# Optimization experiments

Hardware: AMD Instinct MI355X
Metric: run time of the kernel (lower is better)

The kernel has to match this reference:

```python
import jax, jax.numpy as jnp
import numpy as np

N, A, C, H, W = 2, 9, 80, 100, 152
STRIDE = 8
IM_H, IM_W = float(H * STRIDE), float(W * STRIDE)
PRE_NMS_THRESH = 0.05
PRE_NMS_TOP_N = 1000
NMS_THRESH = 0.5
POST_TOP_N = 100
MIN_SIZE = 0.0
WX = WY = 10.0
WW = WH = 5.0
BBOX_XFORM_CLIP = float(np.log(1000.0 / 16.0))
CLS_OFFSET = 4096.0  # > max image coord, makes per-class NMS equivalent


def _make_anchors():
    # 3 scales x 3 ratios, base size 32 at stride 8 (FPN P3)
    sizes = 32.0 * np.array([1.0, 2.0 ** (1.0 / 3.0), 2.0 ** (2.0 / 3.0)])
    ratios = np.array([0.5, 1.0, 2.0])
    ws, hs = [], []
    for s in sizes:
        for r in ratios:
            ws.append(s * np.sqrt(1.0 / r))
            hs.append(s * np.sqrt(r))
    ws = np.array(ws)  # [A]
    hs = np.array(hs)
    sx = (np.arange(W) + 0.5) * STRIDE
    sy = (np.arange(H) + 0.5) * STRIDE
    cx, cy = np.meshgrid(sx, sy)  # [H, W]
    cx = cx.reshape(-1, 1)
    cy = cy.reshape(-1, 1)
    x1 = cx - 0.5 * ws
    y1 = cy - 0.5 * hs
    x2 = cx + 0.5 * ws
    y2 = cy + 0.5 * hs
    # layout matches permute_and_flatten: index = (h*W + w)*A + a
    return np.stack([x1, y1, x2, y2], -1).reshape(-1, 4).astype(np.float32)


def setup_inputs() -> dict:
    key = jax.random.key(0)
    k1, k2 = jax.random.split(key)
    # shift logits down so sigmoid scores are mostly below pre_nms_thresh (realistic sparsity)
    box_cls = jax.random.normal(k1, (N, A * C, H, W), dtype=jnp.float32) * 2.0 - 4.0
    box_regression = jax.random.normal(k2, (N, A * 4, H, W), dtype=jnp.float32)
    anchors = jnp.asarray(_make_anchors())  # [H*W*A, 4]
    return {"box_cls": box_cls, "box_regression": box_regression, "anchors": anchors}


def _decode(rel, anc):
    # BoxCoder(weights=(10,10,5,5)).decode, TO_REMOVE = 1
    widths = anc[..., 2] - anc[..., 0] + 1.0
    heights = anc[..., 3] - anc[..., 1] + 1.0
    ctr_x = anc[..., 0] + 0.5 * widths
    ctr_y = anc[..., 1] + 0.5 * heights
    dx = rel[..., 0] / WX
    dy = rel[..., 1] / WY
    dw = jnp.minimum(rel[..., 2] / WW, BBOX_XFORM_CLIP)
    dh = jnp.minimum(rel[..., 3] / WH, BBOX_XFORM_CLIP)
    pcx = dx * widths + ctr_x
    pcy = dy * heights + ctr_y
    pw = jnp.exp(dw) * widths
    ph = jnp.exp(dh) * heights
    return jnp.stack(
        [pcx - 0.5 * pw, pcy - 0.5 * ph, pcx + 0.5 * pw - 1.0, pcy + 0.5 * ph - 1.0], -1)


def _nms_keep(boxes, scores, valid):
    # greedy NMS over boxes already sorted by score desc; returns bool keep [K]
    x1, y1, x2, y2 = boxes[:, 0], boxes[:, 1], boxes[:, 2], boxes[:, 3]
    areas = (x2 - x1 + 1.0) * (y2 - y1 + 1.0)
    iw = jnp.maximum(jnp.minimum(x2[:, None], x2[None, :]) - jnp.maximum(x1[:, None], x1[None, :]) + 1.0, 0.0)
    ih = jnp.maximum(jnp.minimum(y2[:, None], y2[None, :]) - jnp.maximum(y1[:, None], y1[None, :]) + 1.0, 0.0)
    inter = iw * ih
    iou = inter / (areas[:, None] + areas[None, :] - inter)  # [K, K]
    K = boxes.shape[0]

    def step(supp, i):
        ki = valid[i] & jnp.logical_not(supp[i])
        supp = supp | jnp.where(ki, iou[i] > NMS_THRESH, False)
        return supp, ki

    _, keep = jax.lax.scan(step, jnp.zeros(K, dtype=bool), jnp.arange(K))
    return keep


def reference(box_cls, box_regression, anchors):
    n = box_cls.shape[0]
    # permute_and_flatten: [N, A*C, H, W] -> [N, H*W*A, C], then sigmoid
    scores = jax.nn.sigmoid(
        box_cls.reshape(n, A, C, H, W).transpose(0, 3, 4, 1, 2).reshape(n, H * W * A, C))
    regs = box_regression.reshape(n, A, 4, H, W).transpose(0, 3, 4, 1, 2).reshape(n, H * W * A, 4)
    # threshold + capped top-k over flattened (anchor, class) pairs
    masked = jnp.where(scores > PRE_NMS_THRESH, scores, -1.0).reshape(n, -1)
    top_scores, top_idx = jax.lax.top_k(masked, PRE_NMS_TOP_N)  # sorted desc
    loc = top_idx // C            # anchor location
    labels = top_idx % C + 1      # per_class += 1
    valid = top_scores > 0.0      # padded slots have score -1
    reg_sel = jnp.take_along_axis(regs, loc[..., None], axis=1)  # [N, K, 4]
    anc_sel = anchors[loc]                                       # [N, K, 4]
    boxes = _decode(reg_sel, anc_sel)
    # clip_to_image
    x1 = jnp.clip(boxes[..., 0], 0.0, IM_W - 1.0)
    y1 = jnp.clip(boxes[..., 1], 0.0, IM_H - 1.0)
    x2 = jnp.clip(boxes[..., 2], 0.0, IM_W - 1.0)
    y2 = jnp.clip(boxes[..., 3], 0.0, IM_H - 1.0)
    boxes = jnp.stack([x1, y1, x2, y2], -1)
    # remove_small_boxes (TO_REMOVE = 1)
    valid = valid & (x2 - x1 + 1.0 >= MIN_SIZE) & (y2 - y1 + 1.0 >= MIN_SIZE)
    # per-class NMS via class-offset trick (boxes of different classes never overlap)
    off = labels.astype(boxes.dtype)[..., None] * CLS_OFFSET
    keep = jax.vmap(_nms_keep)(boxes + off, top_scores, valid)
    kept_scores = jnp.where(keep & valid, top_scores, -1.0)
    # select_over_all_levels: keep top fpn_post_nms_top_n by score
    final_scores, fidx = jax.lax.top_k(kept_scores, POST_TOP_N)
    final_boxes = jnp.take_along_axis(boxes, fidx[..., None], axis=1)
    final_labels = jnp.where(final_scores > 0.0, jnp.take_along_axis(labels, fidx, axis=1), 0)
    return final_boxes, final_scores, final_labels
```

## Files before the change

kernel.cpp:

```cpp
#include <hip/hip_runtime.h>


#define W_    152
#define H_    100
#define A_    9
#define C_    80
#define HW_   (H_*W_)
#define PER_IMG  (A_*C_*HW_)
#define PER_IMG4 (PER_IMG/4)
#define NBIN  2048
#define BIGA_CAP 4096
#define SORTN 2048
#define FASTN 1024
#define NDEC  256
#define THRB 2.0f
#define THRA 3.65f
#define CLIPV 4.135166556742356f

#define TPB      256
#define F4_BATCH 16
#define NBATCH   2
#define CHUNK    (TPB*F4_BATCH*NBATCH)
#define NB_SCAN  ((PER_IMG4 + CHUNK - 1) / CHUNK)
#define LCAPA 64

#define OFF_CNTA 0
#define OFF_DONE 8
#define OFF_DEC  256
#define OFF_BIGA (256 + 24576)

typedef unsigned long long u64;

__global__ __launch_bounds__(TPB) void scan_kernel(
    const float* __restrict__ cls,
    unsigned int* __restrict__ cntA,
    u64* __restrict__ bigA) {
  const int n = blockIdx.y;
  const float4* __restrict__ in = reinterpret_cast<const float4*>(cls) + (size_t)n * PER_IMG4;
  __shared__ unsigned int lcntA, lbaseA;
  __shared__ u64 lkA[LCAPA];
  if (threadIdx.x == 0) lcntA = 0;
  __syncthreads();

#pragma unroll
  for (int half = 0; half < NBATCH; ++half) {
    const int hbase = blockIdx.x * CHUNK + half * (TPB * F4_BATCH) + threadIdx.x;
    float4 v[F4_BATCH];
#pragma unroll
    for (int j = 0; j < F4_BATCH; ++j) {
      const int t = hbase + j * TPB;
      v[j] = (t < PER_IMG4) ? in[t]
                            : make_float4(-100.f, -100.f, -100.f, -100.f);
    }
#pragma unroll
    for (int j = 0; j < F4_BATCH; ++j) {
      const float4 vv = v[j];
      const float mx = fmaxf(fmaxf(vv.x, vv.y), fmaxf(vv.z, vv.w));
      if (mx > THRA) {
        const int f0  = (hbase + j * TPB) * 4;
        const int ac  = f0 / HW_;
        const int rem = f0 - ac * HW_;
        const int h   = rem / W_;
        const int w0  = rem - h * W_;
        const int a   = ac / C_;
        const int c   = ac - a * C_;
        const int idx0 = ((h * W_ + w0) * A_ + a) * C_ + c;
        const float xs[4] = {vv.x, vv.y, vv.z, vv.w};
#pragma unroll
        for (int e = 0; e < 4; ++e) {
          const float x = xs[e];
          if (x > THRA) {
            float s = 1.0f / (1.0f + expf(-x));
            unsigned pa = atomicAdd(&lcntA, 1u);
            if (pa < LCAPA)
              lkA[pa] = ((u64)__float_as_uint(s) << 32) |
                        (u64)(0xFFFFFFFFu - (unsigned)(idx0 + e * 720));
          }
        }
      }
    }
  }
  __syncthreads();
  if (threadIdx.x == 0) {
    unsigned cA = lcntA; if (cA > LCAPA) cA = LCAPA;
    lbaseA = cA ? atomicAdd(&cntA[n], cA) : 0u;
    lcntA = cA;
  }
  __syncthreads();
  if (threadIdx.x < lcntA) {
    unsigned pos = lbaseA + threadIdx.x;
    if (pos < BIGA_CAP)
      bigA[(size_t)n * BIGA_CAP + pos] = lkA[threadIdx.x];
  }
}

__device__ __forceinline__ void decode_box(
    int idx, float sc, int n,
    const float* __restrict__ reg, const float* __restrict__ anchors,
    float4& o0, float4& o1, float4& o2) {
  int c   = idx % C_;
  int loc = idx / C_;
  int a   = loc % A_;
  int hw  = loc / A_;
  int hh  = hw / W_;
  int ww  = hw - hh * W_;
  int rb  = ((n * A_ + a) * 4) * HW_ + hh * W_ + ww;
  float r0 = reg[rb], r1 = reg[rb + HW_], r2 = reg[rb + 2*HW_], r3 = reg[rb + 3*HW_];
  float4 an = reinterpret_cast<const float4*>(anchors)[loc];
  float wdt = an.z - an.x + 1.0f, hgt = an.w - an.y + 1.0f;
  float cx  = an.x + 0.5f * wdt, cy = an.y + 0.5f * hgt;
  float dx = r0 / 10.0f, dy = r1 / 10.0f;
  float dw = fminf(r2 / 5.0f, CLIPV), dh = fminf(r3 / 5.0f, CLIPV);
  float pcx = dx * wdt + cx, pcy = dy * hgt + cy;
  float pw = expf(dw) * wdt, ph = expf(dh) * hgt;
  float x1 = pcx - 0.5f * pw, y1 = pcy - 0.5f * ph;
  float x2 = pcx + 0.5f * pw - 1.0f, y2 = pcy + 0.5f * ph - 1.0f;
  x1 = fminf(fmaxf(x1, 0.0f), (float)(W_*8) - 1.0f);
  y1 = fminf(fmaxf(y1, 0.0f), (float)(H_*8) - 1.0f);
  x2 = fminf(fmaxf(x2, 0.0f), (float)(W_*8) - 1.0f);
  y2 = fminf(fmaxf(y2, 0.0f), (float)(H_*8) - 1.0f);
  bool valid = sc > 0.0f;
  if ((x2 - x1 + 1.0f < 0.0f) || (y2 - y1 + 1.0f < 0.0f)) valid = false;
  int   label = c + 1;
  float off = (float)label * 4096.0f;
  float ox1 = x1 + off, oy1 = y1 + off, ox2 = x2 + off, oy2 = y2 + off;
  o0 = make_float4(ox1, oy1, ox2, oy2);
  o1 = make_float4(x1, y1, x2, y2);
  o2 = make_float4((ox2 - ox1 + 1.0f) * (oy2 - oy1 + 1.0f),
                   valid ? sc : -1.0f, (float)label, 0.0f);
}

__global__ __launch_bounds__(256) void rank_nms_kernel(
    const float* __restrict__ cls,
    const unsigned int* __restrict__ cntA,
    const u64* __restrict__ bigA,
    const float* __restrict__ reg, const float* __restrict__ anchors,
    unsigned int* __restrict__ done,
    float4* __restrict__ dec,
    float* __restrict__ out) {
  const int n = blockIdx.x >> 5;
  const int b = blockIdx.x & 31;
  const int tid = threadIdx.x;
  const int lane = tid & 63;

  __shared__ u64 skl[FASTN];
  __shared__ int s_last;
  __shared__ float4 dall[3 * NDEC];
  __shared__ int s_fb, s_k, s_cut, s_cnt;
  __shared__ int keptidx[100];
  __shared__ u64 skey[SORTN];
  __shared__ unsigned int shist[NBIN];
  __shared__ unsigned int csum[256];
  __shared__ float4 fb0[1000], fb1[1000], fb2[1000];
  __shared__ unsigned char skeep[1000];

  const int caRaw = (int)cntA[n];
  int ca = caRaw; if (ca > FASTN) ca = FASTN;

#pragma unroll
  for (int r = 0; r < 4; ++r) {
    int j = tid + r * 256;
    skl[j] = (j < ca) ? bigA[(size_t)n * BIGA_CAP + j] : 0ull;
  }
  __syncthreads();

  const int kidx = b * 32 + (tid >> 3);
  const int sub  = tid & 7;
  const u64 ki = skl[kidx];
  int rank = 0;
#pragma unroll 8
  for (int it = 0; it < 128; ++it) {
    int j = sub + it * 8;
    u64 kj = skl[j];
    rank += (int)((kj > ki) | ((kj == ki) & (j < kidx)));
  }
  rank += __shfl_xor(rank, 1);
  rank += __shfl_xor(rank, 2);
  rank += __shfl_xor(rank, 4);
  if (sub == 0 && rank < NDEC && ki != 0ull) {
    int idx = (int)(0xFFFFFFFFu - (unsigned)(ki & 0xFFFFFFFFu));
    float sc = __uint_as_float((unsigned)(ki >> 32));
    float4 o0, o1, o2;
    decode_box(idx, sc, n, reg, anchors, o0, o1, o2);
    float4* d = dec + (size_t)n * (3 * NDEC);
    d[rank]            = o0;
    d[NDEC + rank]     = o1;
    d[2 * NDEC + rank] = o2;
  }

  __threadfence();
  if (tid == 0) {
    unsigned old = atomicAdd(&done[n], 1u);
    s_last = (old == 31u) ? 1 : 0;
  }
  __syncthreads();
  if (!s_last) return;
  __threadfence();

  if (tid == 0) { s_cnt = 0; s_fb = (caRaw > FASTN || caRaw < NDEC) ? 1 : 0; }

  if (caRaw >= NDEC && caRaw <= FASTN) {
#pragma unroll
    for (int r = 0; r < 3; ++r)
      dall[tid + r * 256] = dec[(size_t)n * (3 * NDEC) + tid + r * 256];
  }
  __syncthreads();

  float4* d0 = dall;
  float4* d1 = dall + NDEC;
  float4* d2 = dall + 2 * NDEC;

  if (s_fb == 0) {
    if (tid < 64) {
      float ka_x1 = 0, ka_y1 = 0, ka_x2 = 0, ka_y2 = 0, ka_ar = 0;
      float kb_x1 = 0, kb_y1 = 0, kb_x2 = 0, kb_y2 = 0, kb_ar = 0;
      int k = 0;
      for (int i = 0; i < NDEC; ++i) {
        if (k >= 100) break;
        float4 bx = d0[i];
        float4 ai = d2[i];
        float x1 = bx.x, y1 = bx.y, x2 = bx.z, y2 = bx.w, ar = ai.x, sc = ai.y;
        bool sup = false;
        if (lane < k) {
          float iw = fminf(x2, ka_x2) - fmaxf(x1, ka_x1) + 1.0f;
          float ih = fminf(y2, ka_y2) - fmaxf(y1, ka_y1) + 1.0f;
          if (iw > 0.0f && ih > 0.0f) {
            float inter = iw * ih;
            sup = inter / (ar + ka_ar - inter) > 0.5f;
          }
        }
        if (lane + 64 < k) {
          float iw = fminf(x2, kb_x2) - fmaxf(x1, kb_x1) + 1.0f;
          float ih = fminf(y2, kb_y2) - fmaxf(y1, kb_y1) + 1.0f;
          if (iw > 0.0f && ih > 0.0f) {
            float inter = iw * ih;
            sup = sup || (inter / (ar + kb_ar - inter) > 0.5f);
          }
        }
        bool any = __any(sup);
        if ((sc > 0.0f) && !any) {
          if (lane == k)      { ka_x1 = x1; ka_y1 = y1; ka_x2 = x2; ka_y2 = y2; ka_ar = ar; }
          if (lane == k - 64) { kb_x1 = x1; kb_y1 = y1; kb_x2 = x2; kb_y2 = y2; kb_ar = ar; }
          if (lane == 0) keptidx[k] = i;
          ++k;
        }
      }
      if (lane == 0) {
        s_k = k;
        if (k < 100) s_fb = 1;
      }
    }
    __syncthreads();

    if (s_fb == 0) {
      if (tid < 100) {
        int f = keptidx[tid];
        float4 bb = d1[f];
        float4 ai = d2[f];
        int ob = (n * 100 + tid) * 4;
        out[ob + 0] = bb.x; out[ob + 1] = bb.y; out[ob + 2] = bb.z; out[ob + 3] = bb.w;
        out[800  + n * 100 + tid] = ai.y;
        out[1000 + n * 100 + tid] = ai.z;
      }
      return;
    }
  }
  __syncthreads();

  for (int i = tid; i < NBIN; i += 256) shist[i] = 0;
  __syncthreads();
  const float* __restrict__ cn = cls + (size_t)n * PER_IMG;
  for (int e = tid; e < PER_IMG; e += 256) {
    float x = cn[e];
    if (x > THRB) {
      int bb = (int)((x - THRB) * 256.0f); if (bb > NBIN - 1) bb = NBIN - 1;
      atomicAdd(&shist[bb], 1u);
    }
  }
  __syncthreads();
  {
    unsigned int s = 0;
    for (int bb = tid * 8; bb < tid * 8 + 8; ++bb) s += shist[bb];
    csum[tid] = s;
  }
  __syncthreads();
  if (tid == 0) {
    int acc = 0, cut = 0;
    for (int cch = 255; cch >= 0; --cch) {
      int nacc = acc + (int)csum[cch];
      if (nacc >= 1000) {
        int aa = acc;
        for (int bb = cch * 8 + 7; bb >= cch * 8; --bb) { aa += (int)shist[bb]; if (aa >= 1000) { cut = bb; break; } }
        break;
      }
      acc = nacc;
    }
    s_cut = cut;
  }
  __syncthreads();
  const int cut = s_cut;
  for (int e = tid; e < PER_IMG; e += 256) {
    float x = cn[e];
    if (x > THRB) {
      int bb = (int)((x - THRB) * 256.0f); if (bb > NBIN - 1) bb = NBIN - 1;
      if (bb >= cut) {
        int ac2 = e / HW_;
        int rem = e - ac2 * HW_;
        int hh  = rem / W_;
        int ww  = rem - hh * W_;
        int a2  = ac2 / C_;
        int c2  = ac2 - a2 * C_;
        int jidx = ((hh * W_ + ww) * A_ + a2) * C_ + c2;
        float s = 1.0f / (1.0f + expf(-x));
        int pos = atomicAdd(&s_cnt, 1);
        if (pos < SORTN)
          skey[pos] = ((u64)__float_as_uint(s) << 32) |
                      (u64)(0xFFFFFFFFu - (unsigned)jidx);
      }
    }
  }
  __syncthreads();
  int cnt = s_cnt; if (cnt > SORTN) cnt = SORTN;
  for (int p = tid; p < SORTN; p += 256)
    if (p >= cnt) skey[p] = 0ull;
  __syncthreads();
  for (int k = 2; k <= SORTN; k <<= 1) {
    for (int j = k >> 1; j > 0; j >>= 1) {
#pragma unroll
      for (int u = 0; u < 8; ++u) {
        int tt = tid + u * 256;
        int ixj = tt ^ j;
        if (ixj > tt) {
          u64 va = skey[tt], vb = skey[ixj];
          bool asc = ((tt & k) == 0);
          if (asc ? (va > vb) : (va < vb)) { skey[tt] = vb; skey[ixj] = va; }
        }
      }
      __syncthreads();
    }
  }
  for (int i = tid; i < 1000; i += 256) {
    u64 key = skey[SORTN - 1 - i];
    bool ok = (i < cnt) && (key != 0ull);
    int   idx = ok ? (int)(0xFFFFFFFFu - (unsigned)(key & 0xFFFFFFFFu)) : 0;
    float sc  = ok ? __uint_as_float((unsigned)(key >> 32)) : -1.0f;
    float4 o0, o1, o2;
    decode_box(idx, sc, n, reg, anchors, o0, o1, o2);
    fb0[i] = o0; fb1[i] = o1; fb2[i] = o2;
  }
  __syncthreads();
  if (tid < 64) {
    float ka_x1 = 0, ka_y1 = 0, ka_x2 = 0, ka_y2 = 0, ka_ar = 0;
    float kb_x1 = 0, kb_y1 = 0, kb_x2 = 0, kb_y2 = 0, kb_ar = 0;
    int k = 0;
    for (int i = 0; i < 1000; ++i) {
      if (k >= 100) break;
      float4 bx = fb0[i];
      float4 ai = fb2[i];
      float x1 = bx.x, y1 = bx.y, x2 = bx.z, y2 = bx.w, ar = ai.x, sc = ai.y;
      bool sup = false;
      if (lane < k) {
        float iw = fminf(x2, ka_x2) - fmaxf(x1, ka_x1) + 1.0f;
        float ih = fminf(y2, ka_y2) - fmaxf(y1, ka_y1) + 1.0f;
        if (iw > 0.0f && ih > 0.0f) {
          float inter = iw * ih;
          sup = inter / (ar + ka_ar - inter) > 0.5f;
        }
      }
      if (lane + 64 < k) {
        float iw = fminf(x2, kb_x2) - fmaxf(x1, kb_x1) + 1.0f;
        float ih = fminf(y2, kb_y2) - fmaxf(y1, kb_y1) + 1.0f;
        if (iw > 0.0f && ih > 0.0f) {
          float inter = iw * ih;
          sup = sup || (inter / (ar + kb_ar - inter) > 0.5f);
        }
      }
      bool any = __any(sup);
      bool valid = sc > 0.0f;
      if (valid && !any) {
        if (lane == k)      { ka_x1 = x1; ka_y1 = y1; ka_x2 = x2; ka_y2 = y2; ka_ar = ar; }
        if (lane == k - 64) { kb_x1 = x1; kb_y1 = y1; kb_x2 = x2; kb_y2 = y2; kb_ar = ar; }
        if (lane == 0) { keptidx[k] = i; skeep[i] = 1; }
        ++k;
      } else if (lane == 0) {
        skeep[i] = 0;
      }
    }
    if (lane == 0) {
      if (k < 100) {
        int fill = k;
        for (int q = 0; q < 1000 && fill < 100; ++q)
          if (!skeep[q]) keptidx[fill++] = q;
      }
      s_k = k;
    }
  }
  __syncthreads();
  if (tid < 100) {
    int f = keptidx[tid];
    bool isk = tid < s_k;
    float4 bb = fb1[f];
    float sc  = isk ? fb2[f].y : -1.0f;
    float lab = (sc > 0.0f) ? fb2[f].z : 0.0f;
    int ob = (n * 100 + tid) * 4;
    out[ob + 0] = bb.x; out[ob + 1] = bb.y; out[ob + 2] = bb.z; out[ob + 3] = bb.w;
    out[800  + n * 100 + tid] = sc;
    out[1000 + n * 100 + tid] = lab;
  }
}

extern "C" void kernel_launch(void* const* d_in, const int* in_sizes, int n_in,
                              void* d_out, int out_size, void* d_ws, size_t ws_size,
                              hipStream_t stream) {
  const float* cls = (const float*)d_in[0];
  const float* reg = (const float*)d_in[1];
  const float* anc = (const float*)d_in[2];
  float* out = (float*)d_out;
  char* ws = (char*)d_ws;
  unsigned int* cntA = (unsigned int*)(ws + OFF_CNTA);
  unsigned int* done = (unsigned int*)(ws + OFF_DONE);
  float4* dec        = (float4*)(ws + OFF_DEC);
  u64*    bigA       = (u64*)(ws + OFF_BIGA);

  hipMemsetAsync(d_ws, 0, 16, stream);
  dim3 g1(NB_SCAN, 2);
  scan_kernel<<<g1, TPB, 0, stream>>>(cls, cntA, bigA);
  rank_nms_kernel<<<64, 256, 0, stream>>>(cls, cntA, bigA, reg, anc, done, dec, out);
}
```

Baseline: 65.85 us.

## Fuse scan and rank/NMS kernels into one launch with a spin-wait barrier

Merges the threshold scan kernel and the rank/NMS kernel into a single launch. The first 32 blocks per image spin-wait on a global counter until all scan blocks finish, then run the rank, decode and NMS stages. Large fallback shared buffers (histogram, sort keys, decoded boxes) move to global workspace, which shrinks shared memory and raises occupancy for the scan phase. The aim is to remove one kernel launch and the gap between kernels. The cost is a spin-wait that relies on all scan blocks being co-resident or scheduled ahead, plus slower global-memory access and extra fences on the fallback sort path.

```diff
diff --git a/kernel.cpp b/kernel.cpp
--- a/kernel.cpp
+++ b/kernel.cpp
@@ -24,75 +24,16 @@
 #define NB_SCAN  ((PER_IMG4 + CHUNK - 1) / CHUNK)
 #define LCAPA 64
 
-#define OFF_CNTA 0
-#define OFF_DONE 8
-#define OFF_DEC  256
-#define OFF_BIGA (256 + 24576)
+#define OFF_CNTA  0
+#define OFF_SDONE 8
+#define OFF_RDONE 16
+#define OFF_DEC   256
+#define OFF_BIGA  (256 + 24576)
+#define OFF_GSKEY (OFF_BIGA + 65536)
+#define OFF_GHIST (OFF_GSKEY + 32768)
+#define OFF_GFB   (OFF_GHIST + 16384)
 
 typedef unsigned long long u64;
-
-__global__ __launch_bounds__(TPB) void scan_kernel(
-    const float* __restrict__ cls,
-    unsigned int* __restrict__ cntA,
-    u64* __restrict__ bigA) {
-  const int n = blockIdx.y;
-  const float4* __restrict__ in = reinterpret_cast<const float4*>(cls) + (size_t)n * PER_IMG4;
-  __shared__ unsigned int lcntA, lbaseA;
-  __shared__ u64 lkA[LCAPA];
-  if (threadIdx.x == 0) lcntA = 0;
-  __syncthreads();
-
-#pragma unroll
-  for (int half = 0; half < NBATCH; ++half) {
-    const int hbase = blockIdx.x * CHUNK + half * (TPB * F4_BATCH) + threadIdx.x;
-    float4 v[F4_BATCH];
-#pragma unroll
-    for (int j = 0; j < F4_BATCH; ++j) {
-      const int t = hbase + j * TPB;
-      v[j] = (t < PER_IMG4) ? in[t]
-                            : make_float4(-100.f, -100.f, -100.f, -100.f);
-    }
-#pragma unroll
-    for (int j = 0; j < F4_BATCH; ++j) {
-      const float4 vv = v[j];
-      const float mx = fmaxf(fmaxf(vv.x, vv.y), fmaxf(vv.z, vv.w));
-      if (mx > THRA) {
-        const int f0  = (hbase + j * TPB) * 4;
-        const int ac  = f0 / HW_;
-        const int rem = f0 - ac * HW_;
-        const int h   = rem / W_;
-        const int w0  = rem - h * W_;
-        const int a   = ac / C_;
-        const int c   = ac - a * C_;
-        const int idx0 = ((h * W_ + w0) * A_ + a) * C_ + c;
-        const float xs[4] = {vv.x, vv.y, vv.z, vv.w};
-#pragma unroll
-        for (int e = 0; e < 4; ++e) {
-          const float x = xs[e];
-          if (x > THRA) {
-            float s = 1.0f / (1.0f + expf(-x));
-            unsigned pa = atomicAdd(&lcntA, 1u);
-            if (pa < LCAPA)
-              lkA[pa] = ((u64)__float_as_uint(s) << 32) |
-                        (u64)(0xFFFFFFFFu - (unsigned)(idx0 + e * 720));
-          }
-        }
-      }
-    }
-  }
-  __syncthreads();
-  if (threadIdx.x == 0) {
-    unsigned cA = lcntA; if (cA > LCAPA) cA = LCAPA;
-    lbaseA = cA ? atomicAdd(&cntA[n], cA) : 0u;
-    lcntA = cA;
-  }
-  __syncthreads();
-  if (threadIdx.x < lcntA) {
-    unsigned pos = lbaseA + threadIdx.x;
-    if (pos < BIGA_CAP)
-      bigA[(size_t)n * BIGA_CAP + pos] = lkA[threadIdx.x];
-  }
-}
 
 __device__ __forceinline__ void decode_box(
     int idx, float sc, int n,
@@ -130,33 +71,103 @@
                    valid ? sc : -1.0f, (float)label, 0.0f);
 }
 
-__global__ __launch_bounds__(256) void rank_nms_kernel(
+__global__ __launch_bounds__(TPB) void fused_kernel(
     const float* __restrict__ cls,
-    const unsigned int* __restrict__ cntA,
-    const u64* __restrict__ bigA,
-    const float* __restrict__ reg, const float* __restrict__ anchors,
-    unsigned int* __restrict__ done,
+    const float* __restrict__ reg,
+    const float* __restrict__ anchors,
+    unsigned int* __restrict__ cntA,
+    unsigned int* __restrict__ sdone,
+    unsigned int* __restrict__ rdone,
+    u64* __restrict__ bigA,
     float4* __restrict__ dec,
+    u64* __restrict__ g_skey,
+    unsigned int* __restrict__ g_hist,
+    float4* __restrict__ g_fb,
     float* __restrict__ out) {
-  const int n = blockIdx.x >> 5;
-  const int b = blockIdx.x & 31;
+  const int n = blockIdx.y;
+  const int b = blockIdx.x;
   const int tid = threadIdx.x;
   const int lane = tid & 63;
 
   __shared__ u64 skl[FASTN];
-  __shared__ int s_last;
   __shared__ float4 dall[3 * NDEC];
-  __shared__ int s_fb, s_k, s_cut, s_cnt;
+  __shared__ u64 lkA[LCAPA];
+  __shared__ unsigned int lcntA, lbaseA;
+  __shared__ int s_last, s_fb, s_k, s_cut, s_cnt;
   __shared__ int keptidx[100];
-  __shared__ u64 skey[SORTN];
-  __shared__ unsigned int shist[NBIN];
   __shared__ unsigned int csum[256];
-  __shared__ float4 fb0[1000], fb1[1000], fb2[1000];
   __shared__ unsigned char skeep[1000];
+
+  if (tid == 0) lcntA = 0;
+  __syncthreads();
+  {
+    const float4* __restrict__ in = reinterpret_cast<const float4*>(cls) + (size_t)n * PER_IMG4;
+#pragma unroll
+    for (int half = 0; half < NBATCH; ++half) {
+      const int hbase = b * CHUNK + half * (TPB * F4_BATCH) + tid;
+      float4 v[F4_BATCH];
+#pragma unroll
+      for (int j = 0; j < F4_BATCH; ++j) {
+        const int t = hbase + j * TPB;
+        v[j] = (t < PER_IMG4) ? in[t]
+                              : make_float4(-100.f, -100.f, -100.f, -100.f);
+      }
+#pragma unroll
+      for (int j = 0; j < F4_BATCH; ++j) {
+        const float4 vv = v[j];
+        const float mx = fmaxf(fmaxf(vv.x, vv.y), fmaxf(vv.z, vv.w));
+        if (mx > THRA) {
+          const int f0  = (hbase + j * TPB) * 4;
+          const int ac  = f0 / HW_;
+          const int rem = f0 - ac * HW_;
+          const int h   = rem / W_;
+          const int w0  = rem - h * W_;
+          const int a   = ac / C_;
+          const int c   = ac - a * C_;
+          const int idx0 = ((h * W_ + w0) * A_ + a) * C_ + c;
+          const float xs[4] = {vv.x, vv.y, vv.z, vv.w};
+#pragma unroll
+          for (int e = 0; e < 4; ++e) {
+            const float x = xs[e];
+            if (x > THRA) {
+              float s = 1.0f / (1.0f + expf(-x));
+              unsigned pa = atomicAdd(&lcntA, 1u);
+              if (pa < LCAPA)
+                lkA[pa] = ((u64)__float_as_uint(s) << 32) |
+                          (u64)(0xFFFFFFFFu - (unsigned)(idx0 + e * 720));
+            }
+          }
+        }
+      }
+    }
+  }
+  __syncthreads();
+  if (tid == 0) {
+    unsigned cA = lcntA; if (cA > LCAPA) cA = LCAPA;
+    lbaseA = cA ? atomicAdd(&cntA[n], cA) : 0u;
+    lcntA = cA;
+  }
+  __syncthreads();
+  if (tid < lcntA) {
+    unsigned pos = lbaseA + tid;
+    if (pos < BIGA_CAP)
+      bigA[(size_t)n * BIGA_CAP + pos] = lkA[tid];
+  }
+  __threadfence();
+  if (tid == 0) atomicAdd(&sdone[n], 1u);
+  if (b >= 32) return;
+
+  if (tid == 0) {
+    while (__hip_atomic_load(&sdone[n], __ATOMIC_ACQUIRE,
+                             __HIP_MEMORY_SCOPE_AGENT) < (unsigned)NB_SCAN) {
+      __builtin_amdgcn_s_sleep(8);
+    }
+  }
+  __syncthreads();
+  __threadfence();
 
   const int caRaw = (int)cntA[n];
   int ca = caRaw; if (ca > FASTN) ca = FASTN;
-
 #pragma unroll
   for (int r = 0; r < 4; ++r) {
     int j = tid + r * 256;
@@ -187,18 +198,13 @@
     d[NDEC + rank]     = o1;
     d[2 * NDEC + rank] = o2;
   }
-
-  __threadfence();
-  if (tid == 0) {
-    unsigned old = atomicAdd(&done[n], 1u);
-    s_last = (old == 31u) ? 1 : 0;
-  }
+  __threadfence();
+  if (tid == 0) s_last = (atomicAdd(&rdone[n], 1u) == 31u) ? 1 : 0;
   __syncthreads();
   if (!s_last) return;
   __threadfence();
 
   if (tid == 0) { s_cnt = 0; s_fb = (caRaw > FASTN || caRaw < NDEC) ? 1 : 0; }
-
   if (caRaw >= NDEC && caRaw <= FASTN) {
 #pragma unroll
     for (int r = 0; r < 3; ++r)
@@ -267,20 +273,27 @@
   }
   __syncthreads();
 
-  for (int i = tid; i < NBIN; i += 256) shist[i] = 0;
-  __syncthreads();
+  unsigned int* hist = g_hist + n * NBIN;
+  u64*  skey = g_skey + n * SORTN;
+  float4* fb0 = g_fb + (size_t)n * 3000;
+  float4* fb1 = fb0 + 1000;
+  float4* fb2 = fb0 + 2000;
+  for (int i = tid; i < NBIN; i += 256) hist[i] = 0;
+  __syncthreads();
+  __threadfence();
   const float* __restrict__ cn = cls + (size_t)n * PER_IMG;
   for (int e = tid; e < PER_IMG; e += 256) {
     float x = cn[e];
     if (x > THRB) {
       int bb = (int)((x - THRB) * 256.0f); if (bb > NBIN - 1) bb = NBIN - 1;
-      atomicAdd(&shist[bb], 1u);
-    }
-  }
-  __syncthreads();
+      atomicAdd(&hist[bb], 1u);
+    }
+  }
+  __syncthreads();
+  __threadfence();
   {
     unsigned int s = 0;
-    for (int bb = tid * 8; bb < tid * 8 + 8; ++bb) s += shist[bb];
+    for (int bb = tid * 8; bb < tid * 8 + 8; ++bb) s += hist[bb];
     csum[tid] = s;
   }
   __syncthreads();
@@ -290,7 +303,7 @@
       int nacc = acc + (int)csum[cch];
       if (nacc >= 1000) {
         int aa = acc;
-        for (int bb = cch * 8 + 7; bb >= cch * 8; --bb) { aa += (int)shist[bb]; if (aa >= 1000) { cut = bb; break; } }
+        for (int bb = cch * 8 + 7; bb >= cch * 8; --bb) { aa += (int)hist[bb]; if (aa >= 1000) { cut = bb; break; } }
         break;
       }
       acc = nacc;
@@ -320,10 +333,12 @@
     }
   }
   __syncthreads();
+  __threadfence();
   int cnt = s_cnt; if (cnt > SORTN) cnt = SORTN;
   for (int p = tid; p < SORTN; p += 256)
     if (p >= cnt) skey[p] = 0ull;
   __syncthreads();
+  __threadfence();
   for (int k = 2; k <= SORTN; k <<= 1) {
     for (int j = k >> 1; j > 0; j >>= 1) {
 #pragma unroll
@@ -337,6 +352,7 @@
         }
       }
       __syncthreads();
+      __threadfence();
     }
   }
   for (int i = tid; i < 1000; i += 256) {
@@ -349,6 +365,7 @@
     fb0[i] = o0; fb1[i] = o1; fb2[i] = o2;
   }
   __syncthreads();
+  __threadfence();
   if (tid < 64) {
     float ka_x1 = 0, ka_y1 = 0, ka_x2 = 0, ka_y2 = 0, ka_ar = 0;
     float kb_x1 = 0, kb_y1 = 0, kb_x2 = 0, kb_y2 = 0, kb_ar = 0;
@@ -417,13 +434,17 @@
   const float* anc = (const float*)d_in[2];
   float* out = (float*)d_out;
   char* ws = (char*)d_ws;
-  unsigned int* cntA = (unsigned int*)(ws + OFF_CNTA);
-  unsigned int* done = (unsigned int*)(ws + OFF_DONE);
-  float4* dec        = (float4*)(ws + OFF_DEC);
-  u64*    bigA       = (u64*)(ws + OFF_BIGA);
-
-  hipMemsetAsync(d_ws, 0, 16, stream);
-  dim3 g1(NB_SCAN, 2);
-  scan_kernel<<<g1, TPB, 0, stream>>>(cls, cntA, bigA);
-  rank_nms_kernel<<<64, 256, 0, stream>>>(cls, cntA, bigA, reg, anc, done, dec, out);
+  unsigned int* cntA  = (unsigned int*)(ws + OFF_CNTA);
+  unsigned int* sdone = (unsigned int*)(ws + OFF_SDONE);
+  unsigned int* rdone = (unsigned int*)(ws + OFF_RDONE);
+  float4* dec         = (float4*)(ws + OFF_DEC);
+  u64*    bigA        = (u64*)(ws + OFF_BIGA);
+  u64*    g_skey      = (u64*)(ws + OFF_GSKEY);
+  unsigned int* g_hist = (unsigned int*)(ws + OFF_GHIST);
+  float4* g_fb        = (float4*)(ws + OFF_GFB);
+
+  hipMemsetAsync(d_ws, 0, 24, stream);
+  dim3 grid(NB_SCAN, 2);
+  fused_kernel<<<grid, TPB, 0, stream>>>(cls, reg, anc, cntA, sdone, rdone,
+                                         bigA, dec, g_skey, g_hist, g_fb, out);
 }
```

New measurement: 134.2 us. +103.7%, slower.
